# Optimization experiments

Measured on AMD Instinct MI355X. Metric: run time of the kernel, lower is better.

## Reference

```python
import jax, jax.numpy as jnp
import numpy as np

N_NODES = 50000
N_EDGES = 1600000
N_INPUT = 256
HID = 32
OUT = N_INPUT // 2
EPS = 1e-12


def gcn_conv(x, edge_index, W, b):
    # Standard GCNConv: D^{-1/2} (A + I) D^{-1/2} X W + b
    N = x.shape[0]
    loop = jnp.arange(N)
    src = jnp.concatenate([edge_index[0], loop])
    dst = jnp.concatenate([edge_index[1], loop])
    deg = jax.ops.segment_sum(jnp.ones_like(src, dtype=x.dtype), dst, num_segments=N)
    dinv = jax.lax.rsqrt(jnp.maximum(deg, 1.0))  # deg >= 1 due to self-loops
    norm = dinv[src] * dinv[dst]                  # [E+N]
    h = x @ W                                     # [N, out]
    msg = h[src] * norm[:, None]                  # gather + scale
    out = jax.ops.segment_sum(msg, dst, num_segments=N)
    return out + b


def l2_normalize(z):
    n = jnp.linalg.norm(z, axis=1, keepdims=True)
    return z / jnp.maximum(n, EPS)


def setup_inputs() -> dict:
    key = jax.random.key(0)
    ks = jax.random.split(key, 9)
    x = jax.random.normal(ks[0], (N_NODES, N_INPUT), dtype=jnp.float32)
    ei_u = jax.random.randint(ks[1], (2, N_EDGES), 0, N_NODES)
    ei_u2 = jax.random.randint(ks[2], (2, N_EDGES), 0, N_NODES)
    s_in = 1.0 / np.sqrt(N_INPUT)
    s_hid = 1.0 / np.sqrt(HID)
    W_in = jax.random.normal(ks[3], (N_INPUT, HID), dtype=jnp.float32) * s_in
    b_in = jnp.zeros((HID,), dtype=jnp.float32)
    W_hid = jax.random.normal(ks[4], (HID, HID), dtype=jnp.float32) * s_hid
    b_hid = jnp.zeros((HID,), dtype=jnp.float32)
    W_out = jax.random.normal(ks[5], (HID, OUT), dtype=jnp.float32) * s_hid
    b_out = jnp.zeros((OUT,), dtype=jnp.float32)
    return {"x": x, "edge_index_u": ei_u, "edge_index_u2": ei_u2,
            "W_in": W_in, "b_in": b_in, "W_hid": W_hid, "b_hid": b_hid,
            "W_out": W_out, "b_out": b_out}


def reference(x, edge_index_u, edge_index_u2, W_in, b_in, W_hid, b_hid, W_out, b_out):
    # layer 1 on both views
    x1 = gcn_conv(x, edge_index_u, W_in, b_in)
    x2 = gcn_conv(x, edge_index_u2, W_in, b_in)
    sim = jnp.sum(l2_normalize(x1) * l2_normalize(x2), axis=1, keepdims=True)
    mian = x1 + x2 * sim
    sup = x2 + x1 * sim
    # layer 2
    x1 = gcn_conv(mian, edge_index_u, W_hid, b_hid)
    x2 = gcn_conv(sup, edge_index_u2, W_hid, b_hid)
    sim = jnp.sum(l2_normalize(x1) * l2_normalize(x2), axis=1, keepdims=True)
    mian = x1 + x2 * sim
    sup = x2 + x1 * sim
    # layer 3: note both branches use edge_index_u (as in source)
    x1 = gcn_conv(mian, edge_index_u, W_out, b_out)
    x2 = gcn_conv(sup, edge_index_u, W_out, b_out)
    return jnp.concatenate([x1, x2], axis=1)
```

## Files before the change

kernel.cpp:

```cpp
#include <hip/hip_runtime.h>
#include <hip/hip_bf16.h>

#define NN 50000
#define NE 1600000
#define NIN 256
#define HID 32
#define FOUT 128
#define OSTR 256
#define NSB ((NN + 255) / 256)
#define CHUNK 2048
#define NCH ((NE + CHUNK - 1) / CHUNK)

static constexpr float EPS = 1e-12f;

__device__ __forceinline__ float b2f(unsigned short s) {
    return __uint_as_float((unsigned)s << 16);
}
__device__ __forceinline__ unsigned short f2b(float f) {
    unsigned u = __float_as_uint(f);
    u += 0x7FFFu + ((u >> 16) & 1u);
    return (unsigned short)(u >> 16);
}
__device__ __forceinline__ unsigned pack2(float a, float b) {
    return (unsigned)f2b(a) | ((unsigned)f2b(b) << 16);
}

__global__ __launch_bounds__(256) void k_hist(const int* __restrict__ dstA,
                                              const int* __restrict__ dstB,
                                              unsigned* __restrict__ hcA,
                                              unsigned* __restrict__ hcB, int half) {
    __shared__ unsigned h[NSB];
    for (int i = threadIdx.x; i < NSB; i += 256) h[i] = 0u;
    __syncthreads();
    bool sec = blockIdx.x >= half;
    int c = sec ? blockIdx.x - half : blockIdx.x;
    const int* dst = sec ? dstB : dstA;
    unsigned* hc = sec ? hcB : hcA;
    int beg = c * CHUNK, end = min(beg + CHUNK, NE);
    for (int e = beg + (int)threadIdx.x; e < end; e += 256)
        atomicAdd(&h[dst[e] >> 8], 1u);
    __syncthreads();
    for (int i = threadIdx.x; i < NSB; i += 256) hc[(size_t)c * NSB + i] = h[i];
}

__global__ __launch_bounds__(256) void k_cscan(unsigned* __restrict__ hcA,
                                               unsigned* __restrict__ hcB,
                                               unsigned* __restrict__ totA,
                                               unsigned* __restrict__ totB, int half) {
    __shared__ unsigned tile[256];
    __shared__ unsigned carry;
    bool sec = blockIdx.x >= half;
    int sb = sec ? blockIdx.x - half : blockIdx.x;
    unsigned* hc = sec ? hcB : hcA;
    unsigned* tot = sec ? totB : totA;
    if (threadIdx.x == 0) carry = 0u;
    __syncthreads();
    for (int base = 0; base < NCH; base += 256) {
        int c = base + (int)threadIdx.x;
        unsigned v = (c < NCH) ? hc[(size_t)c * NSB + sb] : 0u;
        tile[threadIdx.x] = v;
        __syncthreads();
        for (int off = 1; off < 256; off <<= 1) {
            unsigned t = (threadIdx.x >= (unsigned)off) ? tile[threadIdx.x - off] : 0u;
            __syncthreads();
            tile[threadIdx.x] += t;
            __syncthreads();
        }
        if (c < NCH) hc[(size_t)c * NSB + sb] = carry + tile[threadIdx.x] - v;
        __syncthreads();
        if (threadIdx.x == 0) carry += tile[255];
        __syncthreads();
    }
    if (threadIdx.x == 0) tot[sb] = carry;
}

__global__ __launch_bounds__(256) void k_bscan(const unsigned* __restrict__ totA,
                                               const unsigned* __restrict__ totB,
                                               int* __restrict__ bbA, int* __restrict__ bbB) {
    __shared__ unsigned tile[256];
    const unsigned* tot = blockIdx.x ? totB : totA;
    int* bb = blockIdx.x ? bbB : bbA;
    unsigned v = (threadIdx.x < NSB) ? tot[threadIdx.x] : 0u;
    tile[threadIdx.x] = v;
    __syncthreads();
    for (int off = 1; off < 256; off <<= 1) {
        unsigned t = (threadIdx.x >= (unsigned)off) ? tile[threadIdx.x - off] : 0u;
        __syncthreads();
        tile[threadIdx.x] += t;
        __syncthreads();
    }
    if (threadIdx.x < NSB) bb[threadIdx.x] = (int)(tile[threadIdx.x] - v);
    if (threadIdx.x == 0) bb[NSB] = NE;
}

__global__ __launch_bounds__(256) void k_bin1(const int* __restrict__ srcA,
                                              const int* __restrict__ dstA,
                                              const unsigned* __restrict__ hcA,
                                              const int* __restrict__ bbA,
                                              int* __restrict__ tmpA,
                                              const int* __restrict__ srcB,
                                              const int* __restrict__ dstB,
                                              const unsigned* __restrict__ hcB,
                                              const int* __restrict__ bbB,
                                              int* __restrict__ tmpB, int half) {
    __shared__ unsigned hbase[NSB];
    __shared__ unsigned hcur[NSB];
    __shared__ unsigned hscan[NSB];
    __shared__ unsigned tile[256];
    __shared__ unsigned pay[CHUNK];
    __shared__ unsigned gpos[CHUNK];
    bool sec = blockIdx.x >= half;
    int c = sec ? blockIdx.x - half : blockIdx.x;
    const int* src = sec ? srcB : srcA;
    const int* dst = sec ? dstB : dstA;
    const unsigned* hc = sec ? hcB : hcA;
    const int* bb = sec ? bbB : bbA;
    int* tmp = sec ? tmpB : tmpA;
    for (int i = threadIdx.x; i < NSB; i += 256) {
        hbase[i] = (unsigned)bb[i] + hc[(size_t)c * NSB + i];
        hcur[i] = 0u;
    }
    __syncthreads();
    int beg = c * CHUNK;
    int len = min(CHUNK, NE - beg);
    int d[8], s[8];
#pragma unroll
    for (int j = 0; j < 8; ++j) {
        int idx = j * 256 + (int)threadIdx.x;
        if (idx < len) { d[j] = dst[beg + idx]; s[j] = src[beg + idx]; }
        else d[j] = -1;
    }
#pragma unroll
    for (int j = 0; j < 8; ++j)
        if (d[j] >= 0) atomicAdd(&hcur[d[j] >> 8], 1u);
    __syncthreads();
    unsigned v = (threadIdx.x < NSB) ? hcur[threadIdx.x] : 0u;
    tile[threadIdx.x] = v;
    __syncthreads();
    for (int off = 1; off < 256; off <<= 1) {
        unsigned t = (threadIdx.x >= (unsigned)off) ? tile[threadIdx.x - off] : 0u;
        __syncthreads();
        tile[threadIdx.x] += t;
        __syncthreads();
    }
    if (threadIdx.x < NSB) {
        unsigned excl = tile[threadIdx.x] - v;
        hscan[threadIdx.x] = excl;
        hcur[threadIdx.x] = excl;
    }
    __syncthreads();
#pragma unroll
    for (int j = 0; j < 8; ++j) {
        if (d[j] >= 0) {
            int sb = d[j] >> 8;
            unsigned p = atomicAdd(&hcur[sb], 1u);
            pay[p] = ((unsigned)(d[j] & 255) << 16) | (unsigned)s[j];
            gpos[p] = hbase[sb] + (p - hscan[sb]);
        }
    }
    __syncthreads();
    for (int i = threadIdx.x; i < len; i += 256)
        tmp[gpos[i]] = (int)pay[i];
}

__global__ __launch_bounds__(256) void k_bin2(const int* __restrict__ tmpA,
                                              const int* __restrict__ bbA,
                                              unsigned short* __restrict__ csrA,
                                              unsigned* __restrict__ degA,
                                              float* __restrict__ dinvA,
                                              int* __restrict__ rpA,
                                              const int* __restrict__ tmpB,
                                              const int* __restrict__ bbB,
                                              unsigned short* __restrict__ csrB,
                                              unsigned* __restrict__ degB,
                                              float* __restrict__ dinvB,
                                              int* __restrict__ rpB, int half) {
    __shared__ unsigned cnt[256];
    __shared__ unsigned scan[256];
    __shared__ unsigned curs[256];
    bool sec = blockIdx.x >= half;
    int sb = sec ? blockIdx.x - half : blockIdx.x;
    const int* tmp = sec ? tmpB : tmpA;
    const int* bb = sec ? bbB : bbA;
    unsigned short* csr = sec ? csrB : csrA;
    unsigned* deg = sec ? degB : degA;
    float* dinv = sec ? dinvB : dinvA;
    int* rp = sec ? rpB : rpA;
    int beg = bb[sb], end = bb[sb + 1];
    cnt[threadIdx.x] = 0u;
    __syncthreads();
    for (int e = beg + (int)threadIdx.x; e < end; e += 256)
        atomicAdd(&cnt[(tmp[e] >> 16) & 255], 1u);
    __syncthreads();
    unsigned v = cnt[threadIdx.x];
    scan[threadIdx.x] = v;
    __syncthreads();
    for (int off = 1; off < 256; off <<= 1) {
        unsigned t = (threadIdx.x >= (unsigned)off) ? scan[threadIdx.x - off] : 0u;
        __syncthreads();
        scan[threadIdx.x] += t;
        __syncthreads();
    }
    unsigned excl = scan[threadIdx.x] - v;
    int n = sb * 256 + (int)threadIdx.x;
    if (n < NN) {
        deg[n] = v;
        rp[n] = beg + (int)excl;
        dinv[n] = rsqrtf((float)(v + 1u));
    }
    curs[threadIdx.x] = (unsigned)beg + excl;
    __syncthreads();
    for (int e = beg + (int)threadIdx.x; e < end; e += 256) {
        int p = tmp[e];
        unsigned pos = atomicAdd(&curs[(p >> 16) & 255], 1u);
        csr[pos] = (unsigned short)(p & 0xFFFF);
    }
}

__global__ __launch_bounds__(256) void k_gemm_in(const float* __restrict__ x,
                                                 const float* __restrict__ W,
                                                 const float* __restrict__ dinvU,
                                                 const float* __restrict__ dinvV,
                                                 unsigned short* __restrict__ hU,
                                                 unsigned short* __restrict__ hV, int N) {
    int lane = threadIdx.x & 63;
    int c0 = __builtin_amdgcn_readfirstlane((threadIdx.x >> 6) * 8);
    int row = blockIdx.x * 64 + lane;
    if (row >= N) return;
    const float4* xr = reinterpret_cast<const float4*>(x + (size_t)row * NIN);
    float acc[8];
#pragma unroll
    for (int j = 0; j < 8; ++j) acc[j] = 0.f;
#pragma unroll 4
    for (int k4 = 0; k4 < NIN / 4; ++k4) {
        float4 v = xr[k4];
        const float* Wk = W + k4 * 4 * HID + c0;
#pragma unroll
        for (int j = 0; j < 8; ++j) {
            acc[j] = fmaf(v.x, Wk[j], acc[j]);
            acc[j] = fmaf(v.y, Wk[HID + j], acc[j]);
            acc[j] = fmaf(v.z, Wk[2 * HID + j], acc[j]);
            acc[j] = fmaf(v.w, Wk[3 * HID + j], acc[j]);
        }
    }
    float du = dinvU[row], dw = dinvV[row];
    uint4 wu, wv;
    wu.x = pack2(acc[0] * du, acc[1] * du); wu.y = pack2(acc[2] * du, acc[3] * du);
    wu.z = pack2(acc[4] * du, acc[5] * du); wu.w = pack2(acc[6] * du, acc[7] * du);
    wv.x = pack2(acc[0] * dw, acc[1] * dw); wv.y = pack2(acc[2] * dw, acc[3] * dw);
    wv.z = pack2(acc[4] * dw, acc[5] * dw); wv.w = pack2(acc[6] * dw, acc[7] * dw);
    *reinterpret_cast<uint4*>(hU + (size_t)row * HID + c0) = wu;
    *reinterpret_cast<uint4*>(hV + (size_t)row * HID + c0) = wv;
}

__device__ __forceinline__ void pull_sum(const unsigned short* __restrict__ t,
                                         const unsigned short* __restrict__ csr,
                                         const int* __restrict__ rowptr,
                                         const unsigned* __restrict__ deg,
                                         float* __restrict__ out, int blk, int tid) {
    int node = blk * 32 + tid / 8;
    int q = tid % 8;
    if (node >= NN) return;
    const ushort4* h4 = reinterpret_cast<const ushort4*>(t);
    int beg = rowptr[node];
    int end = beg + (int)deg[node];
    ushort4 sv = h4[(size_t)node * 8 + q];
    float4 acc;
    acc.x = b2f(sv.x); acc.y = b2f(sv.y); acc.z = b2f(sv.z); acc.w = b2f(sv.w);
    int e = beg;
    for (; e + 4 <= end; e += 4) {
        int s0 = csr[e], s1 = csr[e + 1], s2 = csr[e + 2], s3 = csr[e + 3];
        ushort4 v0 = h4[(size_t)s0 * 8 + q];
        ushort4 v1 = h4[(size_t)s1 * 8 + q];
        ushort4 v2 = h4[(size_t)s2 * 8 + q];
        ushort4 v3 = h4[(size_t)s3 * 8 + q];
        acc.x += (b2f(v0.x) + b2f(v1.x)) + (b2f(v2.x) + b2f(v3.x));
        acc.y += (b2f(v0.y) + b2f(v1.y)) + (b2f(v2.y) + b2f(v3.y));
        acc.z += (b2f(v0.z) + b2f(v1.z)) + (b2f(v2.z) + b2f(v3.z));
        acc.w += (b2f(v0.w) + b2f(v1.w)) + (b2f(v2.w) + b2f(v3.w));
    }
    for (; e < end; ++e) {
        ushort4 v0 = h4[(size_t)csr[e] * 8 + q];
        acc.x += b2f(v0.x); acc.y += b2f(v0.y);
        acc.z += b2f(v0.z); acc.w += b2f(v0.w);
    }
    *reinterpret_cast<float4*>(out + (size_t)node * HID + q * 4) = acc;
}

__global__ __launch_bounds__(256) void k_pull_pair(
    const unsigned short* __restrict__ tA, const unsigned short* __restrict__ csrA,
    const int* __restrict__ rpA, const unsigned* __restrict__ degA, float* __restrict__ outA,
    const unsigned short* __restrict__ tB, const unsigned short* __restrict__ csrB,
    const int* __restrict__ rpB, const unsigned* __restrict__ degB, float* __restrict__ outB,
    int nblk) {
    int b = blockIdx.x;
    int xcd = b & 7;
    int blk = (b >> 3) * 4 + (xcd & 3);
    if (blk >= nblk) return;
    if (xcd >= 4) pull_sum(tB, csrB, rpB, degB, outB, blk, threadIdx.x);
    else          pull_sum(tA, csrA, rpA, degA, outA, blk, threadIdx.x);
}

__global__ __launch_bounds__(256) void k_mix1(const float* __restrict__ Su,
                                              const float* __restrict__ Sv,
                                              const float* __restrict__ dinvU,
                                              const float* __restrict__ dinvV,
                                              const float* __restrict__ bias,
                                              unsigned short* __restrict__ Tu,
                                              unsigned short* __restrict__ Tv) {
    int node = blockIdx.x * 256 + threadIdx.x;
    if (node >= NN) return;
    const float4* su4 = reinterpret_cast<const float4*>(Su + (size_t)node * HID);
    const float4* sv4 = reinterpret_cast<const float4*>(Sv + (size_t)node * HID);
    float du = dinvU[node], dw = dinvV[node];
    float a[HID], b[HID];
#pragma unroll
    for (int k4 = 0; k4 < 8; ++k4) {
        float4 u = su4[k4];
        float4 v = sv4[k4];
        a[4 * k4 + 0] = fmaf(u.x, du, bias[4 * k4 + 0]);
        a[4 * k4 + 1] = fmaf(u.y, du, bias[4 * k4 + 1]);
        a[4 * k4 + 2] = fmaf(u.z, du, bias[4 * k4 + 2]);
        a[4 * k4 + 3] = fmaf(u.w, du, bias[4 * k4 + 3]);
        b[4 * k4 + 0] = fmaf(v.x, dw, bias[4 * k4 + 0]);
        b[4 * k4 + 1] = fmaf(v.y, dw, bias[4 * k4 + 1]);
        b[4 * k4 + 2] = fmaf(v.z, dw, bias[4 * k4 + 2]);
        b[4 * k4 + 3] = fmaf(v.w, dw, bias[4 * k4 + 3]);
    }
    float n1 = 0.f, n2 = 0.f, dt = 0.f;
#pragma unroll
    for (int c = 0; c < HID; ++c) {
        n1 = fmaf(a[c], a[c], n1);
        n2 = fmaf(b[c], b[c], n2);
        dt = fmaf(a[c], b[c], dt);
    }
    float sim = dt / (fmaxf(sqrtf(n1), EPS) * fmaxf(sqrtf(n2), EPS));
    uint4* pu = reinterpret_cast<uint4*>(Tu + (size_t)node * HID);
    uint4* pv = reinterpret_cast<uint4*>(Tv + (size_t)node * HID);
#pragma unroll
    for (int g = 0; g < 4; ++g) {
        int c = g * 8;
        uint4 mu, mv;
        mu.x = pack2((a[c+0] + b[c+0] * sim) * du, (a[c+1] + b[c+1] * sim) * du);
        mu.y = pack2((a[c+2] + b[c+2] * sim) * du, (a[c+3] + b[c+3] * sim) * du);
        mu.z = pack2((a[c+4] + b[c+4] * sim) * du, (a[c+5] + b[c+5] * sim) * du);
        mu.w = pack2((a[c+6] + b[c+6] * sim) * du, (a[c+7] + b[c+7] * sim) * du);
        mv.x = pack2((b[c+0] + a[c+0] * sim) * dw, (b[c+1] + a[c+1] * sim) * dw);
        mv.y = pack2((b[c+2] + a[c+2] * sim) * dw, (b[c+3] + a[c+3] * sim) * dw);
        mv.z = pack2((b[c+4] + a[c+4] * sim) * dw, (b[c+5] + a[c+5] * sim) * dw);
        mv.w = pack2((b[c+6] + a[c+6] * sim) * dw, (b[c+7] + a[c+7] * sim) * dw);
        pu[g] = mu;
        pv[g] = mv;
    }
}

__global__ __launch_bounds__(128) void k_hid_mix_pack(const float* __restrict__ Su,
                                                      const float* __restrict__ Sv,
                                                      const float* __restrict__ W,
                                                      const float* __restrict__ bias,
                                                      const float* __restrict__ dinvU,
                                                      const float* __restrict__ dinvV,
                                                      unsigned short* __restrict__ Pa,
                                                      unsigned short* __restrict__ Pb) {
    int node = blockIdx.x * 128 + threadIdx.x;
    if (node >= NN) return;
    const float4* su4 = reinterpret_cast<const float4*>(Su + (size_t)node * HID);
    const float4* sv4 = reinterpret_cast<const float4*>(Sv + (size_t)node * HID);
    float du = dinvU[node], dw = dinvV[node];
    float a[HID], b[HID];
#pragma unroll
    for (int c = 0; c < HID; ++c) { a[c] = 0.f; b[c] = 0.f; }
#pragma unroll
    for (int k4 = 0; k4 < HID / 4; ++k4) {
        float4 u = su4[k4];
        float4 v = sv4[k4];
        const float* Wk = W + k4 * 4 * HID;
#pragma unroll
        for (int c = 0; c < HID; ++c) {
            float w0 = Wk[c], w1 = Wk[HID + c], w2 = Wk[2 * HID + c], w3 = Wk[3 * HID + c];
            a[c] = fmaf(u.x, w0, a[c]); a[c] = fmaf(u.y, w1, a[c]);
            a[c] = fmaf(u.z, w2, a[c]); a[c] = fmaf(u.w, w3, a[c]);
            b[c] = fmaf(v.x, w0, b[c]); b[c] = fmaf(v.y, w1, b[c]);
            b[c] = fmaf(v.z, w2, b[c]); b[c] = fmaf(v.w, w3, b[c]);
        }
    }
#pragma unroll
    for (int c = 0; c < HID; ++c) {
        a[c] = fmaf(a[c], du, bias[c]);
        b[c] = fmaf(b[c], dw, bias[c]);
    }
    float n1 = 0.f, n2 = 0.f, dt = 0.f;
#pragma unroll
    for (int c = 0; c < HID; ++c) {
        n1 = fmaf(a[c], a[c], n1);
        n2 = fmaf(b[c], b[c], n2);
        dt = fmaf(a[c], b[c], dt);
    }
    float sim = dt / (fmaxf(sqrtf(n1), EPS) * fmaxf(sqrtf(n2), EPS));
    uint4* pa = reinterpret_cast<uint4*>(Pa + (size_t)node * HID);
    uint4* pb = reinterpret_cast<uint4*>(Pb + (size_t)node * HID);
#pragma unroll
    for (int g = 0; g < 4; ++g) {
        int c = g * 8;
        uint4 ma, mb;
        ma.x = pack2((a[c+0] + b[c+0] * sim) * du, (a[c+1] + b[c+1] * sim) * du);
        ma.y = pack2((a[c+2] + b[c+2] * sim) * du, (a[c+3] + b[c+3] * sim) * du);
        ma.z = pack2((a[c+4] + b[c+4] * sim) * du, (a[c+5] + b[c+5] * sim) * du);
        ma.w = pack2((a[c+6] + b[c+6] * sim) * du, (a[c+7] + b[c+7] * sim) * du);
        mb.x = pack2((b[c+0] + a[c+0] * sim) * du, (b[c+1] + a[c+1] * sim) * du);
        mb.y = pack2((b[c+2] + a[c+2] * sim) * du, (b[c+3] + a[c+3] * sim) * du);
        mb.z = pack2((b[c+4] + a[c+4] * sim) * du, (b[c+5] + a[c+5] * sim) * du);
        mb.w = pack2((b[c+6] + a[c+6] * sim) * du, (b[c+7] + a[c+7] * sim) * du);
        pa[g] = ma;
        pb[g] = mb;
    }
}

__global__ __launch_bounds__(256) void k_gemm_out2(const float* __restrict__ Qa,
                                                   const float* __restrict__ Qb,
                                                   const float* __restrict__ dinvU,
                                                   const float* __restrict__ W,
                                                   const float* __restrict__ b,
                                                   float* __restrict__ out, int N) {
    int lane = threadIdx.x & 63;
    int c0 = __builtin_amdgcn_readfirstlane((threadIdx.x >> 6) * 32);
    int row = blockIdx.x * 64 + lane;
    if (row >= N) return;
    const float4* qa4 = reinterpret_cast<const float4*>(Qa + (size_t)row * HID);
    const float4* qb4 = reinterpret_cast<const float4*>(Qb + (size_t)row * HID);
    float a1[32], a2[32];
#pragma unroll
    for (int j = 0; j < 32; ++j) { a1[j] = 0.f; a2[j] = 0.f; }
#pragma unroll 2
    for (int k4 = 0; k4 < 8; ++k4) {
        float4 v1 = qa4[k4];
        float4 v2 = qb4[k4];
        const float* Wk = W + (k4 * 4) * FOUT + c0;
#pragma unroll
        for (int j = 0; j < 32; ++j) {
            float w0 = Wk[j], w1 = Wk[FOUT + j], w2 = Wk[2 * FOUT + j], w3 = Wk[3 * FOUT + j];
            a1[j] = fmaf(v1.x, w0, a1[j]); a1[j] = fmaf(v1.y, w1, a1[j]);
            a1[j] = fmaf(v1.z, w2, a1[j]); a1[j] = fmaf(v1.w, w3, a1[j]);
            a2[j] = fmaf(v2.x, w0, a2[j]); a2[j] = fmaf(v2.y, w1, a2[j]);
            a2[j] = fmaf(v2.z, w2, a2[j]); a2[j] = fmaf(v2.w, w3, a2[j]);
        }
    }
    float du = dinvU[row];
    float* o1 = out + (size_t)row * OSTR + c0;
    float* o2 = o1 + FOUT;
#pragma unroll
    for (int q = 0; q < 8; ++q) {
        float4 r1, r2;
        r1.x = fmaf(a1[4*q+0], du, b[c0+4*q+0]); r1.y = fmaf(a1[4*q+1], du, b[c0+4*q+1]);
        r1.z = fmaf(a1[4*q+2], du, b[c0+4*q+2]); r1.w = fmaf(a1[4*q+3], du, b[c0+4*q+3]);
        r2.x = fmaf(a2[4*q+0], du, b[c0+4*q+0]); r2.y = fmaf(a2[4*q+1], du, b[c0+4*q+1]);
        r2.z = fmaf(a2[4*q+2], du, b[c0+4*q+2]); r2.w = fmaf(a2[4*q+3], du, b[c0+4*q+3]);
        *reinterpret_cast<float4*>(o1 + 4 * q) = r1;
        *reinterpret_cast<float4*>(o2 + 4 * q) = r2;
    }
}

extern "C" void kernel_launch(void* const* d_in, const int* in_sizes, int n_in,
                              void* d_out, int out_size, void* d_ws, size_t ws_size,
                              hipStream_t stream) {
    const float* x     = (const float*)d_in[0];
    const int*   ei_u  = (const int*)d_in[1];
    const int*   ei_u2 = (const int*)d_in[2];
    const float* W_in  = (const float*)d_in[3];
    const float* b_in  = (const float*)d_in[4];
    const float* W_hid = (const float*)d_in[5];
    const float* b_hid = (const float*)d_in[6];
    const float* W_out = (const float*)d_in[7];
    const float* b_out = (const float*)d_in[8];
    float* out = (float*)d_out;

    const int* src_u  = ei_u;
    const int* dst_u  = ei_u + NE;
    const int* src_u2 = ei_u2;
    const int* dst_u2 = ei_u2 + NE;

    char* w = (char*)d_ws;
    auto carve = [&](size_t bytes) {
        char* p = w;
        w += (bytes + 255) & ~(size_t)255;
        return p;
    };
    unsigned* hc_u   = (unsigned*)carve((size_t)NCH * NSB * sizeof(unsigned));
    unsigned* hc_u2  = (unsigned*)carve((size_t)NCH * NSB * sizeof(unsigned));
    unsigned* tot_u  = (unsigned*)carve(NSB * sizeof(unsigned));
    unsigned* tot_u2 = (unsigned*)carve(NSB * sizeof(unsigned));
    int*      bb_u   = (int*)carve((NSB + 1) * sizeof(int));
    int*      bb_u2  = (int*)carve((NSB + 1) * sizeof(int));
    unsigned* deg_u  = (unsigned*)carve(NN * sizeof(unsigned));
    unsigned* deg_u2 = (unsigned*)carve(NN * sizeof(unsigned));
    float*    dinv_u  = (float*)carve(NN * sizeof(float));
    float*    dinv_u2 = (float*)carve(NN * sizeof(float));
    int*      rp_u   = (int*)carve(NN * sizeof(int));
    int*      rp_u2  = (int*)carve(NN * sizeof(int));
    unsigned short* csr_u  = (unsigned short*)carve((size_t)NE * sizeof(unsigned short));
    unsigned short* csr_u2 = (unsigned short*)carve((size_t)NE * sizeof(unsigned short));
    unsigned short* hU = (unsigned short*)carve((size_t)NN * HID * sizeof(unsigned short));
    unsigned short* hV = (unsigned short*)carve((size_t)NN * HID * sizeof(unsigned short));
    unsigned short* Tu = (unsigned short*)carve((size_t)NN * HID * sizeof(unsigned short));
    unsigned short* Tv = (unsigned short*)carve((size_t)NN * HID * sizeof(unsigned short));
    unsigned short* Pa = (unsigned short*)carve((size_t)NN * HID * sizeof(unsigned short));
    unsigned short* Pb = (unsigned short*)carve((size_t)NN * HID * sizeof(unsigned short));
    float* Su = (float*)carve((size_t)NN * HID * sizeof(float));
    float* Sv = (float*)carve((size_t)NN * HID * sizeof(float));
    int* tmp_u  = (int*)Su;
    int* tmp_u2 = (int*)Sv;

    const int BLK = 256;
    const int gP32 = (NN + 31) / 32;
    const int nPair = ((gP32 + 3) / 4) * 8;
    const int gR64 = (NN + 63) / 64;
    const int gR128 = (NN + 127) / 128;
    const int gN = (NN + 255) / 256;

    k_hist<<<2 * NCH, BLK, 0, stream>>>(dst_u, dst_u2, hc_u, hc_u2, NCH);
    k_cscan<<<2 * NSB, BLK, 0, stream>>>(hc_u, hc_u2, tot_u, tot_u2, NSB);
    k_bscan<<<2, BLK, 0, stream>>>(tot_u, tot_u2, bb_u, bb_u2);
    k_bin1<<<2 * NCH, BLK, 0, stream>>>(src_u, dst_u, hc_u, bb_u, tmp_u,
                                        src_u2, dst_u2, hc_u2, bb_u2, tmp_u2, NCH);
    k_bin2<<<2 * NSB, BLK, 0, stream>>>(tmp_u, bb_u, csr_u, deg_u, dinv_u, rp_u,
                                        tmp_u2, bb_u2, csr_u2, deg_u2, dinv_u2, rp_u2, NSB);

    k_gemm_in<<<gR64, BLK, 0, stream>>>(x, W_in, dinv_u, dinv_u2, hU, hV, NN);
    k_pull_pair<<<nPair, BLK, 0, stream>>>(hU, csr_u, rp_u, deg_u, Su,
                                           hV, csr_u2, rp_u2, deg_u2, Sv, gP32);
    k_mix1<<<gN, BLK, 0, stream>>>(Su, Sv, dinv_u, dinv_u2, b_in, Tu, Tv);

    k_pull_pair<<<nPair, BLK, 0, stream>>>(Tu, csr_u, rp_u, deg_u, Su,
                                           Tv, csr_u2, rp_u2, deg_u2, Sv, gP32);
    k_hid_mix_pack<<<gR128, 128, 0, stream>>>(Su, Sv, W_hid, b_hid, dinv_u, dinv_u2, Pa, Pb);

    k_pull_pair<<<nPair, BLK, 0, stream>>>(Pa, csr_u, rp_u, deg_u, Su,
                                           Pb, csr_u, rp_u, deg_u, Sv, gP32);
    k_gemm_out2<<<gR64, BLK, 0, stream>>>(Su, Sv, dinv_u, W_out, b_out, out, NN);

    (void)in_sizes; (void)n_in; (void)out_size; (void)ws_size;
}
```

Baseline: 229.3 us.

## Spread dense per-node kernels across more threads per node

Dense per-node kernels are repartitioned so each thread owns fewer output columns. k_gemm_in and k_gemm_out2 move to 512-thread blocks with 4 columns (or one view) per wave, and k_mix1 and k_hid_mix_pack use 8 threads per node with shuffle reductions for the norm and dot terms. k_hid_mix_pack also stages W_hid and the inputs in shared memory. The aim is to cut register pressure and raise occupancy and memory-level parallelism, at the cost of redundant x row reads in gemm_in and extra shuffles and syncs.

```diff
diff --git a/kernel.cpp b/kernel.cpp
--- a/kernel.cpp
+++ b/kernel.cpp
@@ -217,26 +217,24 @@
     }
 }
 
-__global__ __launch_bounds__(256) void k_gemm_in(const float* __restrict__ x,
+__global__ __launch_bounds__(512) void k_gemm_in(const float* __restrict__ x,
                                                  const float* __restrict__ W,
                                                  const float* __restrict__ dinvU,
                                                  const float* __restrict__ dinvV,
                                                  unsigned short* __restrict__ hU,
                                                  unsigned short* __restrict__ hV, int N) {
     int lane = threadIdx.x & 63;
-    int c0 = __builtin_amdgcn_readfirstlane((threadIdx.x >> 6) * 8);
+    int c0 = __builtin_amdgcn_readfirstlane((int)(threadIdx.x >> 6) * 4);
     int row = blockIdx.x * 64 + lane;
     if (row >= N) return;
     const float4* xr = reinterpret_cast<const float4*>(x + (size_t)row * NIN);
-    float acc[8];
-#pragma unroll
-    for (int j = 0; j < 8; ++j) acc[j] = 0.f;
+    float acc[4] = {0.f, 0.f, 0.f, 0.f};
 #pragma unroll 4
     for (int k4 = 0; k4 < NIN / 4; ++k4) {
         float4 v = xr[k4];
         const float* Wk = W + k4 * 4 * HID + c0;
 #pragma unroll
-        for (int j = 0; j < 8; ++j) {
+        for (int j = 0; j < 4; ++j) {
             acc[j] = fmaf(v.x, Wk[j], acc[j]);
             acc[j] = fmaf(v.y, Wk[HID + j], acc[j]);
             acc[j] = fmaf(v.z, Wk[2 * HID + j], acc[j]);
@@ -244,13 +242,11 @@
         }
     }
     float du = dinvU[row], dw = dinvV[row];
-    uint4 wu, wv;
+    uint2 wu, wv;
     wu.x = pack2(acc[0] * du, acc[1] * du); wu.y = pack2(acc[2] * du, acc[3] * du);
-    wu.z = pack2(acc[4] * du, acc[5] * du); wu.w = pack2(acc[6] * du, acc[7] * du);
     wv.x = pack2(acc[0] * dw, acc[1] * dw); wv.y = pack2(acc[2] * dw, acc[3] * dw);
-    wv.z = pack2(acc[4] * dw, acc[5] * dw); wv.w = pack2(acc[6] * dw, acc[7] * dw);
-    *reinterpret_cast<uint4*>(hU + (size_t)row * HID + c0) = wu;
-    *reinterpret_cast<uint4*>(hV + (size_t)row * HID + c0) = wv;
+    *reinterpret_cast<uint2*>(hU + (size_t)row * HID + c0) = wu;
+    *reinterpret_cast<uint2*>(hV + (size_t)row * HID + c0) = wv;
 }
 
 __device__ __forceinline__ void pull_sum(const unsigned short* __restrict__ t,
@@ -308,53 +304,40 @@
                                               const float* __restrict__ bias,
                                               unsigned short* __restrict__ Tu,
                                               unsigned short* __restrict__ Tv) {
-    int node = blockIdx.x * 256 + threadIdx.x;
+    int node = blockIdx.x * 32 + (threadIdx.x >> 3);
+    int q = threadIdx.x & 7;
     if (node >= NN) return;
-    const float4* su4 = reinterpret_cast<const float4*>(Su + (size_t)node * HID);
-    const float4* sv4 = reinterpret_cast<const float4*>(Sv + (size_t)node * HID);
+    float4 su = *reinterpret_cast<const float4*>(Su + (size_t)node * HID + 4 * q);
+    float4 sv = *reinterpret_cast<const float4*>(Sv + (size_t)node * HID + 4 * q);
     float du = dinvU[node], dw = dinvV[node];
-    float a[HID], b[HID];
-#pragma unroll
-    for (int k4 = 0; k4 < 8; ++k4) {
-        float4 u = su4[k4];
-        float4 v = sv4[k4];
-        a[4 * k4 + 0] = fmaf(u.x, du, bias[4 * k4 + 0]);
-        a[4 * k4 + 1] = fmaf(u.y, du, bias[4 * k4 + 1]);
-        a[4 * k4 + 2] = fmaf(u.z, du, bias[4 * k4 + 2]);
-        a[4 * k4 + 3] = fmaf(u.w, du, bias[4 * k4 + 3]);
-        b[4 * k4 + 0] = fmaf(v.x, dw, bias[4 * k4 + 0]);
-        b[4 * k4 + 1] = fmaf(v.y, dw, bias[4 * k4 + 1]);
-        b[4 * k4 + 2] = fmaf(v.z, dw, bias[4 * k4 + 2]);
-        b[4 * k4 + 3] = fmaf(v.w, dw, bias[4 * k4 + 3]);
-    }
-    float n1 = 0.f, n2 = 0.f, dt = 0.f;
-#pragma unroll
-    for (int c = 0; c < HID; ++c) {
-        n1 = fmaf(a[c], a[c], n1);
-        n2 = fmaf(b[c], b[c], n2);
-        dt = fmaf(a[c], b[c], dt);
+    float a0 = fmaf(su.x, du, bias[4 * q + 0]);
+    float a1 = fmaf(su.y, du, bias[4 * q + 1]);
+    float a2 = fmaf(su.z, du, bias[4 * q + 2]);
+    float a3 = fmaf(su.w, du, bias[4 * q + 3]);
+    float b0 = fmaf(sv.x, dw, bias[4 * q + 0]);
+    float b1 = fmaf(sv.y, dw, bias[4 * q + 1]);
+    float b2 = fmaf(sv.z, dw, bias[4 * q + 2]);
+    float b3 = fmaf(sv.w, dw, bias[4 * q + 3]);
+    float n1 = a0 * a0 + a1 * a1 + a2 * a2 + a3 * a3;
+    float n2 = b0 * b0 + b1 * b1 + b2 * b2 + b3 * b3;
+    float dt = a0 * b0 + a1 * b1 + a2 * b2 + a3 * b3;
+#pragma unroll
+    for (int m = 4; m >= 1; m >>= 1) {
+        n1 += __shfl_xor(n1, m);
+        n2 += __shfl_xor(n2, m);
+        dt += __shfl_xor(dt, m);
     }
     float sim = dt / (fmaxf(sqrtf(n1), EPS) * fmaxf(sqrtf(n2), EPS));
-    uint4* pu = reinterpret_cast<uint4*>(Tu + (size_t)node * HID);
-    uint4* pv = reinterpret_cast<uint4*>(Tv + (size_t)node * HID);
-#pragma unroll
-    for (int g = 0; g < 4; ++g) {
-        int c = g * 8;
-        uint4 mu, mv;
-        mu.x = pack2((a[c+0] + b[c+0] * sim) * du, (a[c+1] + b[c+1] * sim) * du);
-        mu.y = pack2((a[c+2] + b[c+2] * sim) * du, (a[c+3] + b[c+3] * sim) * du);
-        mu.z = pack2((a[c+4] + b[c+4] * sim) * du, (a[c+5] + b[c+5] * sim) * du);
-        mu.w = pack2((a[c+6] + b[c+6] * sim) * du, (a[c+7] + b[c+7] * sim) * du);
-        mv.x = pack2((b[c+0] + a[c+0] * sim) * dw, (b[c+1] + a[c+1] * sim) * dw);
-        mv.y = pack2((b[c+2] + a[c+2] * sim) * dw, (b[c+3] + a[c+3] * sim) * dw);
-        mv.z = pack2((b[c+4] + a[c+4] * sim) * dw, (b[c+5] + a[c+5] * sim) * dw);
-        mv.w = pack2((b[c+6] + a[c+6] * sim) * dw, (b[c+7] + a[c+7] * sim) * dw);
-        pu[g] = mu;
-        pv[g] = mv;
-    }
-}
-
-__global__ __launch_bounds__(128) void k_hid_mix_pack(const float* __restrict__ Su,
+    uint2 mu, mv;
+    mu.x = pack2((a0 + b0 * sim) * du, (a1 + b1 * sim) * du);
+    mu.y = pack2((a2 + b2 * sim) * du, (a3 + b3 * sim) * du);
+    mv.x = pack2((b0 + a0 * sim) * dw, (b1 + a1 * sim) * dw);
+    mv.y = pack2((b2 + a2 * sim) * dw, (b3 + a3 * sim) * dw);
+    *reinterpret_cast<uint2*>(Tu + (size_t)node * HID + 4 * q) = mu;
+    *reinterpret_cast<uint2*>(Tv + (size_t)node * HID + 4 * q) = mv;
+}
+
+__global__ __launch_bounds__(256) void k_hid_mix_pack(const float* __restrict__ Su,
                                                       const float* __restrict__ Sv,
                                                       const float* __restrict__ W,
                                                       const float* __restrict__ bias,
@@ -362,101 +345,103 @@
                                                       const float* __restrict__ dinvV,
                                                       unsigned short* __restrict__ Pa,
                                                       unsigned short* __restrict__ Pb) {
-    int node = blockIdx.x * 128 + threadIdx.x;
+    __shared__ float Ws[HID * HID];
+    __shared__ float zu[32][33];
+    __shared__ float zv[32][33];
+    int t = threadIdx.x;
+    for (int i = t; i < HID * HID; i += 256) Ws[i] = W[i];
+    int nb = blockIdx.x * 32;
+    int l = t >> 3, q = t & 7;
+    int node = nb + l;
+    {
+        float4 fu = make_float4(0.f, 0.f, 0.f, 0.f), fv = fu;
+        if (node < NN) {
+            fu = *reinterpret_cast<const float4*>(Su + (size_t)node * HID + 4 * q);
+            fv = *reinterpret_cast<const float4*>(Sv + (size_t)node * HID + 4 * q);
+        }
+        zu[l][4 * q + 0] = fu.x; zu[l][4 * q + 1] = fu.y;
+        zu[l][4 * q + 2] = fu.z; zu[l][4 * q + 3] = fu.w;
+        zv[l][4 * q + 0] = fv.x; zv[l][4 * q + 1] = fv.y;
+        zv[l][4 * q + 2] = fv.z; zv[l][4 * q + 3] = fv.w;
+    }
+    __syncthreads();
     if (node >= NN) return;
-    const float4* su4 = reinterpret_cast<const float4*>(Su + (size_t)node * HID);
-    const float4* sv4 = reinterpret_cast<const float4*>(Sv + (size_t)node * HID);
+    float a[4] = {0.f, 0.f, 0.f, 0.f};
+    float b[4] = {0.f, 0.f, 0.f, 0.f};
+#pragma unroll
+    for (int k = 0; k < HID; ++k) {
+        float zuk = zu[l][k], zvk = zv[l][k];
+        const float* Wk = Ws + k * HID + 4 * q;
+#pragma unroll
+        for (int j = 0; j < 4; ++j) {
+            a[j] = fmaf(zuk, Wk[j], a[j]);
+            b[j] = fmaf(zvk, Wk[j], b[j]);
+        }
+    }
     float du = dinvU[node], dw = dinvV[node];
-    float a[HID], b[HID];
-#pragma unroll
-    for (int c = 0; c < HID; ++c) { a[c] = 0.f; b[c] = 0.f; }
-#pragma unroll
-    for (int k4 = 0; k4 < HID / 4; ++k4) {
-        float4 u = su4[k4];
-        float4 v = sv4[k4];
-        const float* Wk = W + k4 * 4 * HID;
-#pragma unroll
-        for (int c = 0; c < HID; ++c) {
-            float w0 = Wk[c], w1 = Wk[HID + c], w2 = Wk[2 * HID + c], w3 = Wk[3 * HID + c];
-            a[c] = fmaf(u.x, w0, a[c]); a[c] = fmaf(u.y, w1, a[c]);
-            a[c] = fmaf(u.z, w2, a[c]); a[c] = fmaf(u.w, w3, a[c]);
-            b[c] = fmaf(v.x, w0, b[c]); b[c] = fmaf(v.y, w1, b[c]);
-            b[c] = fmaf(v.z, w2, b[c]); b[c] = fmaf(v.w, w3, b[c]);
-        }
-    }
-#pragma unroll
-    for (int c = 0; c < HID; ++c) {
-        a[c] = fmaf(a[c], du, bias[c]);
-        b[c] = fmaf(b[c], dw, bias[c]);
-    }
-    float n1 = 0.f, n2 = 0.f, dt = 0.f;
-#pragma unroll
-    for (int c = 0; c < HID; ++c) {
-        n1 = fmaf(a[c], a[c], n1);
-        n2 = fmaf(b[c], b[c], n2);
-        dt = fmaf(a[c], b[c], dt);
+#pragma unroll
+    for (int j = 0; j < 4; ++j) {
+        a[j] = fmaf(a[j], du, bias[4 * q + j]);
+        b[j] = fmaf(b[j], dw, bias[4 * q + j]);
+    }
+    float n1 = a[0]*a[0] + a[1]*a[1] + a[2]*a[2] + a[3]*a[3];
+    float n2 = b[0]*b[0] + b[1]*b[1] + b[2]*b[2] + b[3]*b[3];
+    float dt = a[0]*b[0] + a[1]*b[1] + a[2]*b[2] + a[3]*b[3];
+#pragma unroll
+    for (int m = 4; m >= 1; m >>= 1) {
+        n1 += __shfl_xor(n1, m);
+        n2 += __shfl_xor(n2, m);
+        dt += __shfl_xor(dt, m);
     }
     float sim = dt / (fmaxf(sqrtf(n1), EPS) * fmaxf(sqrtf(n2), EPS));
-    uint4* pa = reinterpret_cast<uint4*>(Pa + (size_t)node * HID);
-    uint4* pb = reinterpret_cast<uint4*>(Pb + (size_t)node * HID);
-#pragma unroll
-    for (int g = 0; g < 4; ++g) {
-        int c = g * 8;
-        uint4 ma, mb;
-        ma.x = pack2((a[c+0] + b[c+0] * sim) * du, (a[c+1] + b[c+1] * sim) * du);
-        ma.y = pack2((a[c+2] + b[c+2] * sim) * du, (a[c+3] + b[c+3] * sim) * du);
-        ma.z = pack2((a[c+4] + b[c+4] * sim) * du, (a[c+5] + b[c+5] * sim) * du);
-        ma.w = pack2((a[c+6] + b[c+6] * sim) * du, (a[c+7] + b[c+7] * sim) * du);
-        mb.x = pack2((b[c+0] + a[c+0] * sim) * du, (b[c+1] + a[c+1] * sim) * du);
-        mb.y = pack2((b[c+2] + a[c+2] * sim) * du, (b[c+3] + a[c+3] * sim) * du);
-        mb.z = pack2((b[c+4] + a[c+4] * sim) * du, (b[c+5] + a[c+5] * sim) * du);
-        mb.w = pack2((b[c+6] + a[c+6] * sim) * du, (b[c+7] + a[c+7] * sim) * du);
-        pa[g] = ma;
-        pb[g] = mb;
-    }
-}
-
-__global__ __launch_bounds__(256) void k_gemm_out2(const float* __restrict__ Qa,
+    uint2 ma, mb;
+    ma.x = pack2((a[0] + b[0] * sim) * du, (a[1] + b[1] * sim) * du);
+    ma.y = pack2((a[2] + b[2] * sim) * du, (a[3] + b[3] * sim) * du);
+    mb.x = pack2((b[0] + a[0] * sim) * du, (b[1] + a[1] * sim) * du);
+    mb.y = pack2((b[2] + a[2] * sim) * du, (b[3] + a[3] * sim) * du);
+    *reinterpret_cast<uint2*>(Pa + (size_t)node * HID + 4 * q) = ma;
+    *reinterpret_cast<uint2*>(Pb + (size_t)node * HID + 4 * q) = mb;
+}
+
+__global__ __launch_bounds__(512) void k_gemm_out2(const float* __restrict__ Qa,
                                                    const float* __restrict__ Qb,
                                                    const float* __restrict__ dinvU,
                                                    const float* __restrict__ W,
                                                    const float* __restrict__ b,
                                                    float* __restrict__ out, int N) {
     int lane = threadIdx.x & 63;
-    int c0 = __builtin_amdgcn_readfirstlane((threadIdx.x >> 6) * 32);
+    int wv = (int)(threadIdx.x >> 6);
+    int view = __builtin_amdgcn_readfirstlane(wv >> 2);
+    int c0 = __builtin_amdgcn_readfirstlane((wv & 3) * 32);
     int row = blockIdx.x * 64 + lane;
     if (row >= N) return;
-    const float4* qa4 = reinterpret_cast<const float4*>(Qa + (size_t)row * HID);
-    const float4* qb4 = reinterpret_cast<const float4*>(Qb + (size_t)row * HID);
-    float a1[32], a2[32];
-#pragma unroll
-    for (int j = 0; j < 32; ++j) { a1[j] = 0.f; a2[j] = 0.f; }
+    const float* Q = view ? Qb : Qa;
+    const float4* q4 = reinterpret_cast<const float4*>(Q + (size_t)row * HID);
+    float a[32];
+#pragma unroll
+    for (int j = 0; j < 32; ++j) a[j] = 0.f;
 #pragma unroll 2
     for (int k4 = 0; k4 < 8; ++k4) {
-        float4 v1 = qa4[k4];
-        float4 v2 = qb4[k4];
+        float4 v = q4[k4];
         const float* Wk = W + (k4 * 4) * FOUT + c0;
 #pragma unroll
         for (int j = 0; j < 32; ++j) {
-            float w0 = Wk[j], w1 = Wk[FOUT + j], w2 = Wk[2 * FOUT + j], w3 = Wk[3 * FOUT + j];
-            a1[j] = fmaf(v1.x, w0, a1[j]); a1[j] = fmaf(v1.y, w1, a1[j]);
-            a1[j] = fmaf(v1.z, w2, a1[j]); a1[j] = fmaf(v1.w, w3, a1[j]);
-            a2[j] = fmaf(v2.x, w0, a2[j]); a2[j] = fmaf(v2.y, w1, a2[j]);
-            a2[j] = fmaf(v2.z, w2, a2[j]); a2[j] = fmaf(v2.w, w3, a2[j]);
+            a[j] = fmaf(v.x, Wk[j], a[j]);
+            a[j] = fmaf(v.y, Wk[FOUT + j], a[j]);
+            a[j] = fmaf(v.z, Wk[2 * FOUT + j], a[j]);
+            a[j] = fmaf(v.w, Wk[3 * FOUT + j], a[j]);
         }
     }
     float du = dinvU[row];
-    float* o1 = out + (size_t)row * OSTR + c0;
-    float* o2 = o1 + FOUT;
-#pragma unroll
-    for (int q = 0; q < 8; ++q) {
-        float4 r1, r2;
-        r1.x = fmaf(a1[4*q+0], du, b[c0+4*q+0]); r1.y = fmaf(a1[4*q+1], du, b[c0+4*q+1]);
-        r1.z = fmaf(a1[4*q+2], du, b[c0+4*q+2]); r1.w = fmaf(a1[4*q+3], du, b[c0+4*q+3]);
-        r2.x = fmaf(a2[4*q+0], du, b[c0+4*q+0]); r2.y = fmaf(a2[4*q+1], du, b[c0+4*q+1]);
-        r2.z = fmaf(a2[4*q+2], du, b[c0+4*q+2]); r2.w = fmaf(a2[4*q+3], du, b[c0+4*q+3]);
-        *reinterpret_cast<float4*>(o1 + 4 * q) = r1;
-        *reinterpret_cast<float4*>(o2 + 4 * q) = r2;
+    float* o = out + (size_t)row * OSTR + view * FOUT + c0;
+#pragma unroll
+    for (int g = 0; g < 8; ++g) {
+        float4 r;
+        r.x = fmaf(a[4*g+0], du, b[c0+4*g+0]);
+        r.y = fmaf(a[4*g+1], du, b[c0+4*g+1]);
+        r.z = fmaf(a[4*g+2], du, b[c0+4*g+2]);
+        r.w = fmaf(a[4*g+3], du, b[c0+4*g+3]);
+        *reinterpret_cast<float4*>(o + 4 * g) = r;
     }
 }
 
@@ -514,8 +499,6 @@
     const int gP32 = (NN + 31) / 32;
     const int nPair = ((gP32 + 3) / 4) * 8;
     const int gR64 = (NN + 63) / 64;
-    const int gR128 = (NN + 127) / 128;
-    const int gN = (NN + 255) / 256;
 
     k_hist<<<2 * NCH, BLK, 0, stream>>>(dst_u, dst_u2, hc_u, hc_u2, NCH);
     k_cscan<<<2 * NSB, BLK, 0, stream>>>(hc_u, hc_u2, tot_u, tot_u2, NSB);
@@ -525,18 +508,18 @@
     k_bin2<<<2 * NSB, BLK, 0, stream>>>(tmp_u, bb_u, csr_u, deg_u, dinv_u, rp_u,
                                         tmp_u2, bb_u2, csr_u2, deg_u2, dinv_u2, rp_u2, NSB);
 
-    k_gemm_in<<<gR64, BLK, 0, stream>>>(x, W_in, dinv_u, dinv_u2, hU, hV, NN);
+    k_gemm_in<<<gR64, 512, 0, stream>>>(x, W_in, dinv_u, dinv_u2, hU, hV, NN);
     k_pull_pair<<<nPair, BLK, 0, stream>>>(hU, csr_u, rp_u, deg_u, Su,
                                            hV, csr_u2, rp_u2, deg_u2, Sv, gP32);
-    k_mix1<<<gN, BLK, 0, stream>>>(Su, Sv, dinv_u, dinv_u2, b_in, Tu, Tv);
+    k_mix1<<<gP32, BLK, 0, stream>>>(Su, Sv, dinv_u, dinv_u2, b_in, Tu, Tv);
 
     k_pull_pair<<<nPair, BLK, 0, stream>>>(Tu, csr_u, rp_u, deg_u, Su,
                                            Tv, csr_u2, rp_u2, deg_u2, Sv, gP32);
-    k_hid_mix_pack<<<gR128, 128, 0, stream>>>(Su, Sv, W_hid, b_hid, dinv_u, dinv_u2, Pa, Pb);
+    k_hid_mix_pack<<<gP32, BLK, 0, stream>>>(Su, Sv, W_hid, b_hid, dinv_u, dinv_u2, Pa, Pb);
 
     k_pull_pair<<<nPair, BLK, 0, stream>>>(Pa, csr_u, rp_u, deg_u, Su,
                                            Pb, csr_u, rp_u, deg_u, Sv, gP32);
-    k_gemm_out2<<<gR64, BLK, 0, stream>>>(Su, Sv, dinv_u, W_out, b_out, out, NN);
+    k_gemm_out2<<<gR64, 512, 0, stream>>>(Su, Sv, dinv_u, W_out, b_out, out, NN);
 
     (void)in_sizes; (void)n_in; (void)out_size; (void)ws_size;
 }
```

After: 247.2 us. +7.8%, slower.
